# Kernel tuning notes

Hardware: AMD Instinct MI355X
Metric: run time of the kernel (lower is better)

## Reference

```python
import jax, jax.numpy as jnp
import numpy as np

N, E, G = 50000, 400000, 500
F_IN, D_H, D_EMB = 92, 256, 128
EPS = 1e-5

def _ln(x, g, b):
    # per-node LayerNorm over feature dim
    mu = jnp.mean(x, axis=-1, keepdims=True)
    var = jnp.mean(jnp.square(x - mu), axis=-1, keepdims=True)
    return (x - mu) * jax.lax.rsqrt(var + EPS) * g + b

def _gcn_conv(x, src, dst, W, b):
    # PyG GCNConv: add self-loops, symmetric normalization
    xw = x @ W                                    # [N, D_out]
    loop = jnp.arange(N, dtype=src.dtype)
    s = jnp.concatenate([src, loop])              # [E+N]
    d = jnp.concatenate([dst, loop])
    deg = jax.ops.segment_sum(jnp.ones_like(d, dtype=xw.dtype), d, num_segments=N)
    dinv = jnp.where(deg > 0, jax.lax.rsqrt(jnp.maximum(deg, 1.0)) * (deg > 0), 0.0)
    norm = dinv[s] * dinv[d]                      # [E+N]
    msg = xw[s] * norm[:, None]                   # gather + scale
    out = jax.ops.segment_sum(msg, d, num_segments=N)  # scatter-add
    return out + b

def setup_inputs() -> dict:
    key = jax.random.key(0)
    ks = jax.random.split(key, 12)
    def lin(k, fan_in, fan_out):
        bound = 1.0 / np.sqrt(fan_in)
        kw, kb = jax.random.split(k)
        W = jax.random.uniform(kw, (fan_in, fan_out), jnp.float32, -bound, bound)
        b = jax.random.uniform(kb, (fan_out,), jnp.float32, -bound, bound)
        return W, b
    x = jax.random.normal(ks[0], (N, F_IN), jnp.float32)
    edge_index = jax.random.randint(ks[1], (2, E), 0, N, jnp.int32)
    batch = jnp.sort(jax.random.randint(ks[2], (N,), 0, G, jnp.int32))
    nfc_W, nfc_b = lin(ks[3], F_IN, D_H)
    gc1_W, gc1_b = lin(ks[4], D_H, D_H)
    gc2_W, gc2_b = lin(ks[5], D_H, D_EMB)
    fc1_W, fc1_b = lin(ks[6], D_EMB, 64)
    fc2_W, fc2_b = lin(ks[7], 64, 1)
    return {
        "x": x, "edge_index": edge_index, "batch": batch,
        "nfc_W": nfc_W, "nfc_b": nfc_b,
        "gn1_g": jnp.ones((D_H,), jnp.float32), "gn1_b": jnp.zeros((D_H,), jnp.float32),
        "gc1_W": gc1_W, "gc1_b": gc1_b,
        "gn2_g": jnp.ones((D_EMB,), jnp.float32), "gn2_b": jnp.zeros((D_EMB,), jnp.float32),
        "gc2_W": gc2_W, "gc2_b": gc2_b,
        "fc1_W": fc1_W, "fc1_b": fc1_b,
        "fc2_W": fc2_W, "fc2_b": fc2_b,
    }

def reference(x, edge_index, batch, nfc_W, nfc_b, gn1_g, gn1_b, gc1_W, gc1_b,
              gn2_g, gn2_b, gc2_W, gc2_b, fc1_W, fc1_b, fc2_W, fc2_b):
    src, dst = edge_index[0], edge_index[1]
    lrelu = jax.nn.leaky_relu  # slope 0.01, matches F.leaky_relu default
    ha = lrelu(x @ nfc_W + nfc_b)
    ha = lrelu(_ln(_gcn_conv(ha, src, dst, gc1_W, gc1_b), gn1_g, gn1_b))
    ha = lrelu(_ln(_gcn_conv(ha, src, dst, gc2_W, gc2_b), gn2_g, gn2_b))
    # F.normalize(p=2, dim=1)
    ha = ha / jnp.maximum(jnp.linalg.norm(ha, axis=1, keepdims=True), 1e-12)
    hg = jax.ops.segment_sum(ha, batch, num_segments=G)   # global_add_pool
    h = lrelu(hg @ fc1_W + fc1_b)
    out = h @ fc2_W + fc2_b
    return out, ha
```

## Files before the change

### kernel.cpp

```cpp
#include <hip/hip_runtime.h>

#define NN 50000
#define EE 400000
#define GG 500
#define F_IN 92
#define KP1 96
#define D_H 256
#define D_EMB 128
#define PCH 16

typedef __attribute__((ext_vector_type(8))) short short8_t;
typedef __attribute__((ext_vector_type(4))) float floatx4;
typedef unsigned short u16;
typedef unsigned int u32;

__device__ __forceinline__ float lrelu(float v) { return v > 0.f ? v : 0.01f * v; }
__device__ __forceinline__ u16 f2b(float v) {
    union { float f; u32 u; } x; x.f = v;
    u32 r = x.u + 0x7FFFu + ((x.u >> 16) & 1u);
    return (u16)(r >> 16);
}
__device__ __forceinline__ float wave_allsum(float v) {
#pragma unroll
    for (int m = 1; m < 64; m <<= 1) v += __shfl_xor(v, m);
    return v;
}
__device__ __forceinline__ void glds16(const void* g, void* l) {
    __builtin_amdgcn_global_load_lds(
        (const __attribute__((address_space(1))) void*)g,
        (__attribute__((address_space(3))) void*)l, 16, 0, 0);
}

__global__ void count_kernel(const int* __restrict__ dst, int* __restrict__ cnt, int E) {
    int e = blockIdx.x * blockDim.x + threadIdx.x;
    if (e < E) atomicAdd(&cnt[dst[e]], 1);
}

__global__ void scan1(const int* __restrict__ cnt, int* __restrict__ excl,
                      int* __restrict__ bsum, float* __restrict__ dinv, int n) {
    __shared__ int sm[256];
    int i = blockIdx.x * 256 + threadIdx.x;
    int v = (i < n) ? cnt[i] : 0;
    if (i < n) dinv[i] = rsqrtf((float)v + 1.0f);
    sm[threadIdx.x] = v;
    __syncthreads();
#pragma unroll
    for (int off = 1; off < 256; off <<= 1) {
        int t = (threadIdx.x >= off) ? sm[threadIdx.x - off] : 0;
        __syncthreads();
        sm[threadIdx.x] += t;
        __syncthreads();
    }
    if (i < n) excl[i] = sm[threadIdx.x] - v;
    if (threadIdx.x == 255) bsum[blockIdx.x] = sm[255];
}
__global__ void scan2(int* __restrict__ bsum, int nb) {
    __shared__ int sm[256];
    int v = (threadIdx.x < nb) ? bsum[threadIdx.x] : 0;
    sm[threadIdx.x] = v;
    __syncthreads();
#pragma unroll
    for (int off = 1; off < 256; off <<= 1) {
        int t = (threadIdx.x >= off) ? sm[threadIdx.x - off] : 0;
        __syncthreads();
        sm[threadIdx.x] += t;
        __syncthreads();
    }
    if (threadIdx.x < nb) bsum[threadIdx.x] = sm[threadIdx.x] - v;
}
__global__ void scan3(int* __restrict__ rowptr, const int* __restrict__ bsum, int n, int E) {
    int i = blockIdx.x * 256 + threadIdx.x;
    if (i < n) rowptr[i] += bsum[blockIdx.x];
    if (i == 0) rowptr[n] = E;
}

__global__ void scatter_kernel(const int* __restrict__ src, const int* __restrict__ dst,
                               const int* __restrict__ rowptr, int* __restrict__ cursor,
                               int* __restrict__ esrc, int E) {
    int e = blockIdx.x * blockDim.x + threadIdx.x;
    if (e >= E) return;
    int d = dst[e];
    int p = rowptr[d] + atomicAdd(&cursor[d], 1);
    esrc[p] = src[e];
}

#define WN_ELEMS (D_H * KP1)
#define W1_ELEMS (D_H * D_H)
#define W2_ELEMS (D_EMB * D_H)
__global__ void cast_all(const float* __restrict__ nfc_W, const float* __restrict__ gc1_W,
                         const float* __restrict__ gc2_W, u16* __restrict__ WtN,
                         u16* __restrict__ Wt1, u16* __restrict__ Wt2) {
    int i = blockIdx.x * blockDim.x + threadIdx.x;
    if (i < WN_ELEMS) {
        int n = i / KP1, k = i % KP1;
        WtN[i] = f2b(k < F_IN ? nfc_W[(long)k * D_H + n] : 0.f);
    } else if (i < WN_ELEMS + W1_ELEMS) {
        int j = i - WN_ELEMS;
        int n = j / D_H, k = j % D_H;
        Wt1[j] = f2b(gc1_W[(long)k * D_H + n]);
    } else if (i < WN_ELEMS + W1_ELEMS + W2_ELEMS) {
        int j = i - WN_ELEMS - W1_ELEMS;
        int n = j / D_H, k = j % D_H;
        Wt2[j] = f2b(gc2_W[(long)k * D_EMB + n]);
    }
}

__global__ __launch_bounds__(256) void gemm_f32a(const float* __restrict__ Af_,
                                                 const u16* __restrict__ Wt,
                                                 const float* __restrict__ bias,
                                                 u16* __restrict__ out,
                                                 int M, int Ka, int Kreal) {
    __shared__ u16 As[128][40];
    __shared__ u16 Bs[256][32];
    int tid = threadIdx.x;
    int wave = tid >> 6, lane = tid & 63;
    int lm = lane & 15, lk = lane >> 4;
    int m0 = blockIdx.x * 128;
    int rowA = tid >> 1, skA = (tid & 1) * 16;
    int lr = lane >> 2, lc = (lane & 3) * 8;
    int gmA = m0 + rowA;
    const float* Af = Af_ + (size_t)gmA * Kreal;
    const u16* Bp[4];
#pragma unroll
    for (int ch = 0; ch < 4; ++ch)
        Bp[ch] = Wt + (size_t)(wave * 64 + ch * 16 + lr) * Ka + lc;
    floatx4 acc[2][16] = {};
    for (int k0 = 0; k0 < Ka; k0 += 32) {
        float f[16];
#pragma unroll
        for (int q = 0; q < 4; ++q) {
            int col = k0 + skA + 4 * q;
            float4 t = make_float4(0.f, 0.f, 0.f, 0.f);
            if (gmA < M && col < Kreal) t = *(const float4*)(Af + col);
            f[4 * q] = t.x; f[4 * q + 1] = t.y; f[4 * q + 2] = t.z; f[4 * q + 3] = t.w;
        }
        u32 pk[8];
#pragma unroll
        for (int t2 = 0; t2 < 8; ++t2)
            pk[t2] = ((u32)f2b(f[2 * t2 + 1]) << 16) | f2b(f[2 * t2]);
        __syncthreads();
        *(uint4*)&As[rowA][skA] = make_uint4(pk[0], pk[1], pk[2], pk[3]);
        *(uint4*)&As[rowA][skA + 8] = make_uint4(pk[4], pk[5], pk[6], pk[7]);
#pragma unroll
        for (int ch = 0; ch < 4; ++ch)
            glds16(Bp[ch] + k0, &Bs[wave * 64 + ch * 16][0]);
        __syncthreads();
        short8_t af0 = *(const short8_t*)&As[wave * 32 + lm][lk * 8];
        short8_t af1 = *(const short8_t*)&As[wave * 32 + 16 + lm][lk * 8];
#pragma unroll
        for (int c = 0; c < 16; ++c) {
            short8_t bf = *(const short8_t*)&Bs[c * 16 + lm][lk * 8];
            acc[0][c] = __builtin_amdgcn_mfma_f32_16x16x32_bf16(af0, bf, acc[0][c], 0, 0, 0);
            acc[1][c] = __builtin_amdgcn_mfma_f32_16x16x32_bf16(af1, bf, acc[1][c], 0, 0, 0);
        }
    }
#pragma unroll
    for (int h = 0; h < 2; ++h) {
#pragma unroll
        for (int r = 0; r < 4; ++r) {
            int gm = m0 + wave * 32 + h * 16 + lk * 4 + r;
            if (gm >= M) continue;
#pragma unroll
            for (int c = 0; c < 16; ++c) {
                int gn = c * 16 + lm;
                float v = acc[h][c][r] + bias[gn];
                out[(size_t)gm * D_H + gn] = f2b(lrelu(v));
            }
        }
    }
}

template <int ND>
__global__ __launch_bounds__(256) void gemm_glds(const u16* __restrict__ A,
                                                 const u16* __restrict__ Wt,
                                                 const float* __restrict__ rscale,
                                                 u16* __restrict__ out,
                                                 int M, int Ka) {
    constexpr int NC  = ND / 16;
    constexpr int BCH = ND / 64;
    __shared__ u16 As[2][128][32];
    __shared__ u16 Bs[2][ND][32];
    int tid = threadIdx.x;
    int wave = tid >> 6, lane = tid & 63;
    int lm = lane & 15, lk = lane >> 4;
    int m0 = blockIdx.x * 128;
    int lr = lane >> 2;
    int lc = (lane & 3) * 8;
    const u16* ApA = A + (size_t)(m0 + wave * 32 + lr) * Ka + lc;
    const u16* ApB = A + (size_t)(m0 + wave * 32 + 16 + lr) * Ka + lc;
    const u16* Bp[BCH];
#pragma unroll
    for (int ch = 0; ch < BCH; ++ch)
        Bp[ch] = Wt + (size_t)(wave * (ND / 4) + ch * 16 + lr) * Ka + lc;

    auto stage = [&](int b, int k0) {
        glds16(ApA + k0, &As[b][wave * 32][0]);
        glds16(ApB + k0, &As[b][wave * 32 + 16][0]);
#pragma unroll
        for (int ch = 0; ch < BCH; ++ch)
            glds16(Bp[ch] + k0, &Bs[b][wave * (ND / 4) + ch * 16][0]);
    };

    floatx4 acc[2][NC] = {};
    int nk = Ka >> 5;
    stage(0, 0);
    asm volatile("s_waitcnt vmcnt(0)" ::: "memory");
    __builtin_amdgcn_s_barrier();
    __builtin_amdgcn_sched_barrier(0);
    int cur = 0;
    for (int t = 0; t < nk; ++t) {
        if (t + 1 < nk) stage(cur ^ 1, (t + 1) * 32);
        short8_t af0 = *(const short8_t*)&As[cur][wave * 32 + lm][lk * 8];
        short8_t af1 = *(const short8_t*)&As[cur][wave * 32 + 16 + lm][lk * 8];
#pragma unroll
        for (int c = 0; c < NC; ++c) {
            short8_t bf = *(const short8_t*)&Bs[cur][c * 16 + lm][lk * 8];
            acc[0][c] = __builtin_amdgcn_mfma_f32_16x16x32_bf16(af0, bf, acc[0][c], 0, 0, 0);
            acc[1][c] = __builtin_amdgcn_mfma_f32_16x16x32_bf16(af1, bf, acc[1][c], 0, 0, 0);
        }
        if (t + 1 < nk) {
            __builtin_amdgcn_sched_barrier(0);
            asm volatile("s_waitcnt vmcnt(0)" ::: "memory");
            __builtin_amdgcn_s_barrier();
            __builtin_amdgcn_sched_barrier(0);
            cur ^= 1;
        }
    }
#pragma unroll
    for (int h = 0; h < 2; ++h) {
#pragma unroll
        for (int r = 0; r < 4; ++r) {
            int gm = m0 + wave * 32 + h * 16 + lk * 4 + r;
            if (gm >= M) continue;
            float rs = rscale[gm];
#pragma unroll
            for (int c = 0; c < NC; ++c) {
                int gn = c * 16 + lm;
                out[(size_t)gm * ND + gn] = f2b(acc[h][c][r] * rs);
            }
        }
    }
}

template <int U>
__device__ __forceinline__ void loadrow(const u32* __restrict__ p, u32* r) {
    if constexpr (U == 2) { uint2 t = *(const uint2*)p; r[0] = t.x; r[1] = t.y; }
    else                  { r[0] = *p; }
}
template <int D, bool L2N, bool TOBF>
__global__ __launch_bounds__(256) void agg_ln(const u16* __restrict__ y,
                                              const int* __restrict__ rowptr,
                                              const int* __restrict__ esrc,
                                              const float* __restrict__ dinv,
                                              const float* __restrict__ bias,
                                              const float* __restrict__ gamma,
                                              const float* __restrict__ beta,
                                              u16* __restrict__ outb,
                                              float* __restrict__ outf) {
    constexpr int V = D / 64;
    constexpr int U = V / 2;
    constexpr int RW = D / 2;
    int wave = threadIdx.x >> 6, lane = threadIdx.x & 63;
    int i = blockIdx.x * 4 + wave;
    if (i >= NN) return;
    int beg = __builtin_amdgcn_readfirstlane(rowptr[i]);
    int end = __builtin_amdgcn_readfirstlane(rowptr[i + 1]);
    const u32* yu = (const u32*)y;
    const int lu = lane * U;
    float accL[U] = {}, accH[U] = {};
    u32 r[8][U];
    int k = beg;
    for (; k + 7 < end; k += 8) {
#pragma unroll
        for (int q = 0; q < 8; ++q) loadrow<U>(yu + (size_t)esrc[k + q] * RW + lu, r[q]);
#pragma unroll
        for (int j = 0; j < U; ++j) {
            float sL = 0.f, sH = 0.f;
#pragma unroll
            for (int q = 0; q < 8; ++q) {
                sL += __uint_as_float(r[q][j] << 16);
                sH += __uint_as_float(r[q][j] & 0xFFFF0000u);
            }
            accL[j] += sL; accH[j] += sH;
        }
    }
    for (; k + 3 < end; k += 4) {
#pragma unroll
        for (int q = 0; q < 4; ++q) loadrow<U>(yu + (size_t)esrc[k + q] * RW + lu, r[q]);
#pragma unroll
        for (int j = 0; j < U; ++j) {
            accL[j] += (__uint_as_float(r[0][j] << 16) + __uint_as_float(r[1][j] << 16))
                     + (__uint_as_float(r[2][j] << 16) + __uint_as_float(r[3][j] << 16));
            accH[j] += (__uint_as_float(r[0][j] & 0xFFFF0000u) + __uint_as_float(r[1][j] & 0xFFFF0000u))
                     + (__uint_as_float(r[2][j] & 0xFFFF0000u) + __uint_as_float(r[3][j] & 0xFFFF0000u));
        }
    }
    for (; k < end; ++k) {
        loadrow<U>(yu + (size_t)esrc[k] * RW + lu, r[0]);
#pragma unroll
        for (int j = 0; j < U; ++j) {
            accL[j] += __uint_as_float(r[0][j] << 16);
            accH[j] += __uint_as_float(r[0][j] & 0xFFFF0000u);
        }
    }
    loadrow<U>(yu + (size_t)i * RW + lu, r[0]);
#pragma unroll
    for (int j = 0; j < U; ++j) {
        accL[j] += __uint_as_float(r[0][j] << 16);
        accH[j] += __uint_as_float(r[0][j] & 0xFFFF0000u);
    }
    float di = dinv[i];
    float xv[V], lsum = 0.f;
#pragma unroll
    for (int j = 0; j < U; ++j) {
        xv[2 * j]     = accL[j] * di + bias[lane * V + 2 * j];
        xv[2 * j + 1] = accH[j] * di + bias[lane * V + 2 * j + 1];
    }
#pragma unroll
    for (int v = 0; v < V; ++v) lsum += xv[v];
    float mu = wave_allsum(lsum) * (1.0f / D);
    float l2 = 0.f;
#pragma unroll
    for (int v = 0; v < V; ++v) { xv[v] -= mu; l2 += xv[v] * xv[v]; }
    float rstd = rsqrtf(wave_allsum(l2) * (1.0f / D) + 1e-5f);
    float yv[V], ss = 0.f;
#pragma unroll
    for (int v = 0; v < V; ++v) {
        float t = xv[v] * rstd * gamma[lane * V + v] + beta[lane * V + v];
        t = lrelu(t);
        yv[v] = t; ss += t * t;
    }
    if constexpr (L2N) {
        float inv = 1.0f / fmaxf(sqrtf(wave_allsum(ss)), 1e-12f);
#pragma unroll
        for (int v = 0; v < V; ++v) yv[v] *= inv;
    }
    if constexpr (TOBF) {
        if constexpr (V == 4) {
            *(ushort4*)(outb + (size_t)i * D + lane * V) =
                make_ushort4(f2b(yv[0]), f2b(yv[1]), f2b(yv[2]), f2b(yv[3]));
        } else {
            *(ushort2*)(outb + (size_t)i * D + lane * V) = make_ushort2(f2b(yv[0]), f2b(yv[1]));
        }
    } else {
        if constexpr (V == 2) {
            *(float2*)(outf + (size_t)i * D + lane * V) = make_float2(yv[0], yv[1]);
        } else {
            *(float4*)(outf + (size_t)i * D + lane * V) = make_float4(yv[0], yv[1], yv[2], yv[3]);
        }
    }
}

__global__ __launch_bounds__(128) void pool_partial(const float* __restrict__ ha,
                                                    const int* __restrict__ batch,
                                                    float* __restrict__ hg) {
    int r0 = blockIdx.x * PCH;
    int f = threadIdx.x;
    int end = min(r0 + PCH, NN);
    int cur = batch[r0];
    float acc = 0.f;
    for (int i = r0; i < end; ++i) {
        int b = batch[i];
        if (b != cur) {
            atomicAdd(&hg[(size_t)cur * D_EMB + f], acc);
            acc = 0.f; cur = b;
        }
        acc += ha[(size_t)i * D_EMB + f];
    }
    atomicAdd(&hg[(size_t)cur * D_EMB + f], acc);
}

__global__ __launch_bounds__(64) void head_kernel(const float* __restrict__ hg,
                                                  const float* __restrict__ fc1W,
                                                  const float* __restrict__ fc1b,
                                                  const float* __restrict__ fc2W,
                                                  const float* __restrict__ fc2b,
                                                  float* __restrict__ out) {
    int g = blockIdx.x;
    int j = threadIdx.x;
    float h = fc1b[j];
#pragma unroll 8
    for (int k = 0; k < D_EMB; ++k) h += hg[(size_t)g * D_EMB + k] * fc1W[k * 64 + j];
    h = lrelu(h) * fc2W[j];
#pragma unroll
    for (int m = 1; m < 64; m <<= 1) h += __shfl_xor(h, m);
    if (j == 0) out[g] = h + fc2b[0];
}

static inline size_t align256(size_t x) { return (x + 255) & ~(size_t)255; }

extern "C" void kernel_launch(void* const* d_in, const int* in_sizes, int n_in,
                              void* d_out, int out_size, void* d_ws, size_t ws_size,
                              hipStream_t stream) {
    const float* x     = (const float*)d_in[0];
    const int*   ei    = (const int*)d_in[1];
    const int*   batch = (const int*)d_in[2];
    const float* nfc_W = (const float*)d_in[3];
    const float* nfc_b = (const float*)d_in[4];
    const float* gn1_g = (const float*)d_in[5];
    const float* gn1_b = (const float*)d_in[6];
    const float* gc1_W = (const float*)d_in[7];
    const float* gc1_b = (const float*)d_in[8];
    const float* gn2_g = (const float*)d_in[9];
    const float* gn2_b = (const float*)d_in[10];
    const float* gc2_W = (const float*)d_in[11];
    const float* gc2_b = (const float*)d_in[12];
    const float* fc1_W = (const float*)d_in[13];
    const float* fc1_b = (const float*)d_in[14];
    const float* fc2_W = (const float*)d_in[15];
    const float* fc2_b = (const float*)d_in[16];

    char* ws = (char*)d_ws;
    size_t off = 0;
    int*   cnt    = (int*)(ws + off);   off += (size_t)NN * 4;
    int*   cursor = (int*)(ws + off);   off += (size_t)NN * 4;
    float* hg     = (float*)(ws + off); off += align256((size_t)GG * D_EMB * 4);
    float* dinv   = (float*)(ws + off); off += align256((size_t)NN * 4);
    int*   rowptr = (int*)(ws + off);   off += align256((size_t)(NN + 1) * 4);
    int*   bsum   = (int*)(ws + off);   off += align256((size_t)256 * 4);
    int*   esrc   = (int*)(ws + off);   off += align256((size_t)EE * 4);
    u16*   WtN    = (u16*)(ws + off);   off += align256((size_t)D_H * KP1 * 2);
    u16*   Wt1    = (u16*)(ws + off);   off += align256((size_t)D_H * D_H * 2);
    u16*   Wt2    = (u16*)(ws + off);   off += align256((size_t)D_EMB * D_H * 2);
    u16*   ha1b   = (u16*)(ws + off);   off += align256((size_t)NN * D_H * 2);
    u16*   y1b    = (u16*)(ws + off);   off += align256((size_t)NN * D_H * 2);
    u16*   ha2b   = (u16*)(ws + off);   off += align256((size_t)NN * D_H * 2);
    u16*   y2b    = (u16*)(ws + off);   off += align256((size_t)NN * D_EMB * 2);

    const int* src = ei;
    const int* dst = ei + EE;
    float* out_scores = (float*)d_out;
    float* out_ha     = (float*)d_out + GG;

    const int NB = (NN + 255) / 256;
    const int MB = (NN + 127) / 128;
    const size_t zbytes = (size_t)NN * 8 + (size_t)GG * D_EMB * 4;

    hipMemsetAsync(cnt, 0, zbytes, stream);
    count_kernel<<<(EE + 255) / 256, 256, 0, stream>>>(dst, cnt, EE);
    scan1<<<NB, 256, 0, stream>>>(cnt, rowptr, bsum, dinv, NN);
    scan2<<<1, 256, 0, stream>>>(bsum, NB);
    scan3<<<NB, 256, 0, stream>>>(rowptr, bsum, NN, EE);
    scatter_kernel<<<(EE + 255) / 256, 256, 0, stream>>>(src, dst, rowptr, cursor, esrc, EE);

    cast_all<<<(WN_ELEMS + W1_ELEMS + W2_ELEMS + 255) / 256, 256, 0, stream>>>(
        nfc_W, gc1_W, gc2_W, WtN, Wt1, Wt2);

    gemm_f32a<<<dim3(MB), 256, 0, stream>>>(x, WtN, nfc_b, ha1b, NN, KP1, F_IN);

    gemm_glds<D_H><<<dim3(MB), 256, 0, stream>>>(ha1b, Wt1, dinv, y1b, NN, D_H);
    agg_ln<D_H, false, true><<<NN / 4, 256, 0, stream>>>(
        y1b, rowptr, esrc, dinv, gc1_b, gn1_g, gn1_b, ha2b, nullptr);

    gemm_glds<D_EMB><<<dim3(MB), 256, 0, stream>>>(ha2b, Wt2, dinv, y2b, NN, D_H);
    agg_ln<D_EMB, true, false><<<NN / 4, 256, 0, stream>>>(
        y2b, rowptr, esrc, dinv, gc2_b, gn2_g, gn2_b, nullptr, out_ha);

    pool_partial<<<(NN + PCH - 1) / PCH, 128, 0, stream>>>(out_ha, batch, hg);
    head_kernel<<<GG, 64, 0, stream>>>(hg, fc1_W, fc1_b, fc2_W, fc2_b, out_scores);
}
```

Before: 291.6 us.

## Fuse CSR build into GEMM launches and pooling into final aggregation

The degree-count atomics now run as extra blocks appended to the first GEMM launch, and the CSR scatter runs as extra blocks in the second GEMM launch, so the graph preprocessing overlaps with dense compute instead of needing its own kernels. The global add pool is folded into the last aggregation kernel: each block reduces its four rows per graph in shared memory before issuing atomics to hg. This removes three kernel launches and a full re-read of the output embeddings. The cost is mixed-workload launches that may hurt GEMM block scheduling, plus an extra shared-memory reduction and barrier in the aggregation kernel.

```diff
diff --git a/kernel.cpp b/kernel.cpp
--- a/kernel.cpp
+++ b/kernel.cpp
@@ -7,7 +7,6 @@
 #define KP1 96
 #define D_H 256
 #define D_EMB 128
-#define PCH 16
 
 typedef __attribute__((ext_vector_type(8))) short short8_t;
 typedef __attribute__((ext_vector_type(4))) float floatx4;
@@ -29,11 +28,6 @@
     __builtin_amdgcn_global_load_lds(
         (const __attribute__((address_space(1))) void*)g,
         (__attribute__((address_space(3))) void*)l, 16, 0, 0);
-}
-
-__global__ void count_kernel(const int* __restrict__ dst, int* __restrict__ cnt, int E) {
-    int e = blockIdx.x * blockDim.x + threadIdx.x;
-    if (e < E) atomicAdd(&cnt[dst[e]], 1);
 }
 
 __global__ void scan1(const int* __restrict__ cnt, int* __restrict__ excl,
@@ -72,16 +66,6 @@
     int i = blockIdx.x * 256 + threadIdx.x;
     if (i < n) rowptr[i] += bsum[blockIdx.x];
     if (i == 0) rowptr[n] = E;
-}
-
-__global__ void scatter_kernel(const int* __restrict__ src, const int* __restrict__ dst,
-                               const int* __restrict__ rowptr, int* __restrict__ cursor,
-                               int* __restrict__ esrc, int E) {
-    int e = blockIdx.x * blockDim.x + threadIdx.x;
-    if (e >= E) return;
-    int d = dst[e];
-    int p = rowptr[d] + atomicAdd(&cursor[d], 1);
-    esrc[p] = src[e];
 }
 
 #define WN_ELEMS (D_H * KP1)
@@ -109,7 +93,14 @@
                                                  const u16* __restrict__ Wt,
                                                  const float* __restrict__ bias,
                                                  u16* __restrict__ out,
-                                                 int M, int Ka, int Kreal) {
+                                                 const int* __restrict__ dstE,
+                                                 int* __restrict__ cnt,
+                                                 int MBLK) {
+    if ((int)blockIdx.x >= MBLK) {
+        int e = (blockIdx.x - MBLK) * 256 + threadIdx.x;
+        if (e < EE) atomicAdd(&cnt[dstE[e]], 1);
+        return;
+    }
     __shared__ u16 As[128][40];
     __shared__ u16 Bs[256][32];
     int tid = threadIdx.x;
@@ -119,19 +110,19 @@
     int rowA = tid >> 1, skA = (tid & 1) * 16;
     int lr = lane >> 2, lc = (lane & 3) * 8;
     int gmA = m0 + rowA;
-    const float* Af = Af_ + (size_t)gmA * Kreal;
+    const float* Af = Af_ + (size_t)gmA * F_IN;
     const u16* Bp[4];
 #pragma unroll
     for (int ch = 0; ch < 4; ++ch)
-        Bp[ch] = Wt + (size_t)(wave * 64 + ch * 16 + lr) * Ka + lc;
+        Bp[ch] = Wt + (size_t)(wave * 64 + ch * 16 + lr) * KP1 + lc;
     floatx4 acc[2][16] = {};
-    for (int k0 = 0; k0 < Ka; k0 += 32) {
+    for (int k0 = 0; k0 < KP1; k0 += 32) {
         float f[16];
 #pragma unroll
         for (int q = 0; q < 4; ++q) {
             int col = k0 + skA + 4 * q;
             float4 t = make_float4(0.f, 0.f, 0.f, 0.f);
-            if (gmA < M && col < Kreal) t = *(const float4*)(Af + col);
+            if (gmA < NN && col < F_IN) t = *(const float4*)(Af + col);
             f[4 * q] = t.x; f[4 * q + 1] = t.y; f[4 * q + 2] = t.z; f[4 * q + 3] = t.w;
         }
         u32 pk[8];
@@ -159,7 +150,7 @@
 #pragma unroll
         for (int r = 0; r < 4; ++r) {
             int gm = m0 + wave * 32 + h * 16 + lk * 4 + r;
-            if (gm >= M) continue;
+            if (gm >= NN) continue;
 #pragma unroll
             for (int c = 0; c < 16; ++c) {
                 int gn = c * 16 + lm;
@@ -170,12 +161,28 @@
     }
 }
 
-template <int ND>
+template <int ND, bool SCAT>
 __global__ __launch_bounds__(256) void gemm_glds(const u16* __restrict__ A,
                                                  const u16* __restrict__ Wt,
                                                  const float* __restrict__ rscale,
                                                  u16* __restrict__ out,
-                                                 int M, int Ka) {
+                                                 const int* __restrict__ srcE,
+                                                 const int* __restrict__ dstE,
+                                                 const int* __restrict__ rowptr,
+                                                 int* __restrict__ cursor,
+                                                 int* __restrict__ esrc,
+                                                 int MBLK) {
+    if constexpr (SCAT) {
+        if ((int)blockIdx.x >= MBLK) {
+            int e = (blockIdx.x - MBLK) * 256 + threadIdx.x;
+            if (e < EE) {
+                int d = dstE[e];
+                int p = rowptr[d] + atomicAdd(&cursor[d], 1);
+                esrc[p] = srcE[e];
+            }
+            return;
+        }
+    }
     constexpr int NC  = ND / 16;
     constexpr int BCH = ND / 64;
     __shared__ u16 As[2][128][32];
@@ -186,6 +193,7 @@
     int m0 = blockIdx.x * 128;
     int lr = lane >> 2;
     int lc = (lane & 3) * 8;
+    const int Ka = D_H;
     const u16* ApA = A + (size_t)(m0 + wave * 32 + lr) * Ka + lc;
     const u16* ApB = A + (size_t)(m0 + wave * 32 + 16 + lr) * Ka + lc;
     const u16* Bp[BCH];
@@ -202,7 +210,7 @@
     };
 
     floatx4 acc[2][NC] = {};
-    int nk = Ka >> 5;
+    constexpr int nk = D_H / 32;
     stage(0, 0);
     asm volatile("s_waitcnt vmcnt(0)" ::: "memory");
     __builtin_amdgcn_s_barrier();
@@ -231,7 +239,7 @@
 #pragma unroll
         for (int r = 0; r < 4; ++r) {
             int gm = m0 + wave * 32 + h * 16 + lk * 4 + r;
-            if (gm >= M) continue;
+            if (gm >= NN) continue;
             float rs = rscale[gm];
 #pragma unroll
             for (int c = 0; c < NC; ++c) {
@@ -247,7 +255,7 @@
     if constexpr (U == 2) { uint2 t = *(const uint2*)p; r[0] = t.x; r[1] = t.y; }
     else                  { r[0] = *p; }
 }
-template <int D, bool L2N, bool TOBF>
+template <int D, bool L2N, bool TOBF, bool POOL>
 __global__ __launch_bounds__(256) void agg_ln(const u16* __restrict__ y,
                                               const int* __restrict__ rowptr,
                                               const int* __restrict__ esrc,
@@ -256,13 +264,15 @@
                                               const float* __restrict__ gamma,
                                               const float* __restrict__ beta,
                                               u16* __restrict__ outb,
-                                              float* __restrict__ outf) {
+                                              float* __restrict__ outf,
+                                              const int* __restrict__ batch,
+                                              float* __restrict__ hg) {
     constexpr int V = D / 64;
     constexpr int U = V / 2;
     constexpr int RW = D / 2;
     int wave = threadIdx.x >> 6, lane = threadIdx.x & 63;
     int i = blockIdx.x * 4 + wave;
-    if (i >= NN) return;
+    if constexpr (!POOL) { if (i >= NN) return; }
     int beg = __builtin_amdgcn_readfirstlane(rowptr[i]);
     int end = __builtin_amdgcn_readfirstlane(rowptr[i + 1]);
     const u32* yu = (const u32*)y;
@@ -349,25 +359,28 @@
             *(float4*)(outf + (size_t)i * D + lane * V) = make_float4(yv[0], yv[1], yv[2], yv[3]);
         }
     }
-}
-
-__global__ __launch_bounds__(128) void pool_partial(const float* __restrict__ ha,
-                                                    const int* __restrict__ batch,
-                                                    float* __restrict__ hg) {
-    int r0 = blockIdx.x * PCH;
-    int f = threadIdx.x;
-    int end = min(r0 + PCH, NN);
-    int cur = batch[r0];
-    float acc = 0.f;
-    for (int i = r0; i < end; ++i) {
-        int b = batch[i];
-        if (b != cur) {
-            atomicAdd(&hg[(size_t)cur * D_EMB + f], acc);
-            acc = 0.f; cur = b;
-        }
-        acc += ha[(size_t)i * D_EMB + f];
-    }
-    atomicAdd(&hg[(size_t)cur * D_EMB + f], acc);
+    if constexpr (POOL) {
+        __shared__ float psm[4][D_EMB];
+        __shared__ int pb[4];
+        psm[wave][lane * 2]     = yv[0];
+        psm[wave][lane * 2 + 1] = yv[1];
+        if (lane == 0) pb[wave] = batch[i];
+        __syncthreads();
+        int tid = threadIdx.x;
+        if (tid < D_EMB) {
+            float acc = psm[0][tid];
+            int cur = pb[0];
+#pragma unroll
+            for (int w = 1; w < 4; ++w) {
+                if (pb[w] != cur) {
+                    atomicAdd(&hg[(size_t)cur * D_EMB + tid], acc);
+                    acc = 0.f; cur = pb[w];
+                }
+                acc += psm[w][tid];
+            }
+            atomicAdd(&hg[(size_t)cur * D_EMB + tid], acc);
+        }
+    }
 }
 
 __global__ __launch_bounds__(64) void head_kernel(const float* __restrict__ hg,
@@ -434,28 +447,28 @@
 
     const int NB = (NN + 255) / 256;
     const int MB = (NN + 127) / 128;
+    const int EB = (EE + 255) / 256;
     const size_t zbytes = (size_t)NN * 8 + (size_t)GG * D_EMB * 4;
 
     hipMemsetAsync(cnt, 0, zbytes, stream);
-    count_kernel<<<(EE + 255) / 256, 256, 0, stream>>>(dst, cnt, EE);
+    cast_all<<<(WN_ELEMS + W1_ELEMS + W2_ELEMS + 255) / 256, 256, 0, stream>>>(
+        nfc_W, gc1_W, gc2_W, WtN, Wt1, Wt2);
+
+    gemm_f32a<<<MB + EB, 256, 0, stream>>>(x, WtN, nfc_b, ha1b, dst, cnt, MB);
+
     scan1<<<NB, 256, 0, stream>>>(cnt, rowptr, bsum, dinv, NN);
     scan2<<<1, 256, 0, stream>>>(bsum, NB);
     scan3<<<NB, 256, 0, stream>>>(rowptr, bsum, NN, EE);
-    scatter_kernel<<<(EE + 255) / 256, 256, 0, stream>>>(src, dst, rowptr, cursor, esrc, EE);
-
-    cast_all<<<(WN_ELEMS + W1_ELEMS + W2_ELEMS + 255) / 256, 256, 0, stream>>>(
-        nfc_W, gc1_W, gc2_W, WtN, Wt1, Wt2);
-
-    gemm_f32a<<<dim3(MB), 256, 0, stream>>>(x, WtN, nfc_b, ha1b, NN, KP1, F_IN);
-
-    gemm_glds<D_H><<<dim3(MB), 256, 0, stream>>>(ha1b, Wt1, dinv, y1b, NN, D_H);
-    agg_ln<D_H, false, true><<<NN / 4, 256, 0, stream>>>(
-        y1b, rowptr, esrc, dinv, gc1_b, gn1_g, gn1_b, ha2b, nullptr);
-
-    gemm_glds<D_EMB><<<dim3(MB), 256, 0, stream>>>(ha2b, Wt2, dinv, y2b, NN, D_H);
-    agg_ln<D_EMB, true, false><<<NN / 4, 256, 0, stream>>>(
-        y2b, rowptr, esrc, dinv, gc2_b, gn2_g, gn2_b, nullptr, out_ha);
-
-    pool_partial<<<(NN + PCH - 1) / PCH, 128, 0, stream>>>(out_ha, batch, hg);
+
+    gemm_glds<D_H, true><<<MB + EB, 256, 0, stream>>>(
+        ha1b, Wt1, dinv, y1b, src, dst, rowptr, cursor, esrc, MB);
+    agg_ln<D_H, false, true, false><<<NN / 4, 256, 0, stream>>>(
+        y1b, rowptr, esrc, dinv, gc1_b, gn1_g, gn1_b, ha2b, nullptr, nullptr, nullptr);
+
+    gemm_glds<D_EMB, false><<<MB, 256, 0, stream>>>(
+        ha2b, Wt2, dinv, y2b, nullptr, nullptr, nullptr, nullptr, nullptr, MB);
+    agg_ln<D_EMB, true, false, true><<<NN / 4, 256, 0, stream>>>(
+        y2b, rowptr, esrc, dinv, gc2_b, gn2_g, gn2_b, nullptr, out_ha, batch, hg);
+
     head_kernel<<<GG, 64, 0, stream>>>(hg, fc1_W, fc1_b, fc2_W, fc2_b, out_scores);
 }
```

New measurement: 253.2 us. 13.2% less time.
